# Kernel optimization log

Measured on AMD Instinct MI355X. Metric: run time of the kernel, lower is better.

## Reference

```python
import jax, jax.numpy as jnp
import numpy as np
import math

B, T, D = 1, 4096, 1024
H = 16
HD = D // H  # 64


def _rotate_half(x):
    d = x.shape[-1] // 2
    return jnp.concatenate([-x[..., d:], x[..., :d]], axis=-1)


def setup_inputs() -> dict:
    key = jax.random.key(0)
    k1, k2, k3 = jax.random.split(key, 3)
    x = jax.random.normal(k1, (B, T, D), dtype=jnp.float32)
    # Linear weights stored as (in, out) so forward is x @ W
    w_qkv = jax.random.normal(k2, (D, 3 * D), dtype=jnp.float32) * (1.0 / math.sqrt(D))
    w_proj = jax.random.normal(k3, (D, D), dtype=jnp.float32) * (1.0 / math.sqrt(D))
    return {"x": x, "w_qkv": w_qkv, "w_proj": w_proj}


def reference(x, w_qkv, w_proj):
    b, t, c = x.shape
    qkv = x @ w_qkv  # [b,t,3c]
    q, k, v = jnp.split(qkv, 3, axis=-1)
    # [b,h,t,hd]
    q = q.reshape(b, t, H, HD).transpose(0, 2, 1, 3)
    k = k.reshape(b, t, H, HD).transpose(0, 2, 1, 3)
    v = v.reshape(b, t, H, HD).transpose(0, 2, 1, 3)

    # RoPE (rotate_half style)
    inv_freq = 1.0 / (10000.0 ** (jnp.arange(0, HD, 2, dtype=jnp.float32) / HD))
    pos = jnp.arange(t, dtype=jnp.float32)
    freqs = jnp.outer(pos, inv_freq)            # [t, hd/2]
    cos = jnp.concatenate([jnp.cos(freqs), jnp.cos(freqs)], axis=-1)[None, None]  # [1,1,t,hd]
    sin = jnp.concatenate([jnp.sin(freqs), jnp.sin(freqs)], axis=-1)[None, None]
    q = q * cos + _rotate_half(q) * sin
    k = k * cos + _rotate_half(k) * sin

    att = jnp.einsum('bhqd,bhkd->bhqk', q, k) / math.sqrt(HD)  # [b,h,t,t]
    causal = jnp.tril(jnp.ones((t, t), dtype=bool))
    att = jnp.where(causal, att, -jnp.inf)
    att = jax.nn.softmax(att, axis=-1)
    # dropout is identity in eval mode
    y = jnp.einsum('bhqk,bhkd->bhqd', att, v)
    y = y.transpose(0, 2, 1, 3).reshape(b, t, c)
    return y @ w_proj
```

## Files before the change

kernel.cpp:

```cpp
#include <hip/hip_runtime.h>
#include <hip/hip_fp16.h>
#include <math.h>

#define TT 4096
#define DD 1024
#define NH 16
#define HD 64

typedef __attribute__((ext_vector_type(8))) _Float16 half8v;
typedef __attribute__((ext_vector_type(4))) _Float16 half4v;
typedef __attribute__((ext_vector_type(4))) float f32x4;

#define GLDS16(g, l)                                                        \
    __builtin_amdgcn_global_load_lds(                                       \
        (const __attribute__((address_space(1))) void*)(g),                 \
        (__attribute__((address_space(3))) void*)(l), 16, 0, 0)

__global__ __launch_bounds__(256) void cast_x(const float* __restrict__ X,
                                              _Float16* __restrict__ Xh)
{
    const int i = (blockIdx.x * 256 + threadIdx.x) * 8;
    float4 a = *(const float4*)&X[i];
    float4 b = *(const float4*)&X[i + 4];
    half8v o = {(_Float16)a.x, (_Float16)a.y, (_Float16)a.z, (_Float16)a.w,
                (_Float16)b.x, (_Float16)b.y, (_Float16)b.z, (_Float16)b.w};
    *(half8v*)&Xh[i] = o;
}

__global__ __launch_bounds__(256) void transpose_cast(
    const float* __restrict__ W, _Float16* __restrict__ WT, int K, int N)
{
    __shared__ float tile[64][65];
    const int t = threadIdx.x;
    const int k0 = blockIdx.y * 64, n0 = blockIdx.x * 64;
    const int c = (t & 15) * 4, r = t >> 4;
#pragma unroll
    for (int i = 0; i < 4; i++) {
        float4 v = *(const float4*)&W[(size_t)(k0 + r + 16 * i) * N + n0 + c];
        tile[r + 16 * i][c + 0] = v.x;
        tile[r + 16 * i][c + 1] = v.y;
        tile[r + 16 * i][c + 2] = v.z;
        tile[r + 16 * i][c + 3] = v.w;
    }
    __syncthreads();
#pragma unroll
    for (int i = 0; i < 4; i++) {
        const int n = r + 16 * i;
        half4v o;
        o[0] = (_Float16)tile[c + 0][n];
        o[1] = (_Float16)tile[c + 1][n];
        o[2] = (_Float16)tile[c + 2][n];
        o[3] = (_Float16)tile[c + 3][n];
        *(half4v*)&WT[(size_t)(n0 + n) * K + k0 + c] = o;
    }
}

template <int MODE>
__global__ __launch_bounds__(256) void gemm_h(
    const _Float16* __restrict__ A, const _Float16* __restrict__ Bt,
    float* __restrict__ C0, _Float16* __restrict__ Q,
    _Float16* __restrict__ Kk, _Float16* __restrict__ V,
    int M, int N, int K)
{
    __shared__ _Float16 As[128 * 32];
    __shared__ _Float16 Bs[128 * 32];
    const int tid  = threadIdx.x;
    const int wave = tid >> 6;
    const int lane = tid & 63;
    const int quad = lane >> 4;
    const int n16  = lane & 15;
    const int n0 = blockIdx.x * 128;
    const int m0 = blockIdx.y * 128;
    const int wr = (wave & 1) * 64;
    const int wc = (wave >> 1) * 64;

    f32x4 acc[4][4];
#pragma unroll
    for (int i = 0; i < 4; i++)
#pragma unroll
        for (int j = 0; j < 4; j++) acc[i][j] = (f32x4){0.f, 0.f, 0.f, 0.f};

    const int srow = tid >> 2;
    const int scol = (tid & 3) * 8;
    const _Float16* Ag = A + (size_t)(m0 + srow) * K + scol;
    const _Float16* Bg = Bt + (size_t)(n0 + srow) * K + scol;
    _Float16* AsW = As + (size_t)wave * 512;
    _Float16* BsW = Bs + (size_t)wave * 512;

    for (int k0 = 0; k0 < K; k0 += 32) {
        __syncthreads();
        GLDS16(Ag + k0, AsW);
        GLDS16(Ag + (size_t)64 * K + k0, AsW + 2048);
        GLDS16(Bg + k0, BsW);
        GLDS16(Bg + (size_t)64 * K + k0, BsW + 2048);
        __syncthreads();

        half8v aF[4], bF[4];
#pragma unroll
        for (int i = 0; i < 4; i++)
            aF[i] = *(const half8v*)&As[(size_t)(wr + i * 16 + n16) * 32 + quad * 8];
#pragma unroll
        for (int j = 0; j < 4; j++)
            bF[j] = *(const half8v*)&Bs[(size_t)(wc + j * 16 + n16) * 32 + quad * 8];
#pragma unroll
        for (int i = 0; i < 4; i++)
#pragma unroll
            for (int j = 0; j < 4; j++)
                acc[i][j] = __builtin_amdgcn_mfma_f32_16x16x32_f16(
                    aF[i], bF[j], acc[i][j], 0, 0, 0);
    }

    if (MODE == 0) {
#pragma unroll
        for (int i = 0; i < 4; i++)
#pragma unroll
            for (int j = 0; j < 4; j++)
#pragma unroll
                for (int r = 0; r < 4; r++) {
                    const int m = m0 + wr + i * 16 + quad * 4 + r;
                    const int n = n0 + wc + j * 16 + n16;
                    C0[(size_t)m * N + n] = acc[i][j][r];
                }
    } else {
        const int ncol0 = n0 + wc;
        const int which = ncol0 >> 10;
        const int h = (ncol0 & 1023) >> 6;
        if (which < 2) {
            _Float16* dst = (which == 0) ? Q : Kk;
            const float sc = (which == 0) ? 0.125f * 1.44269504f : 1.0f;
            const float K2 = 0.4152410118609203f;
#pragma unroll
            for (int jlo = 0; jlo < 2; jlo++) {
                const int d = jlo * 16 + n16;
                const float invf = exp2f(-(float)d * K2);
#pragma unroll
                for (int i = 0; i < 4; i++) {
#pragma unroll
                    for (int r = 0; r < 4; r++) {
                        const int t = m0 + wr + i * 16 + quad * 4 + r;
                        const float f = (float)t * invf;
                        float sn, cs;
                        __sincosf(f, &sn, &cs);
                        const float lo = acc[i][jlo][r];
                        const float hi = acc[i][jlo + 2][r];
                        const size_t off = ((size_t)h * TT + t) * HD + d;
                        dst[off]      = (_Float16)((lo * cs - hi * sn) * sc);
                        dst[off + 32] = (_Float16)((hi * cs + lo * sn) * sc);
                    }
                }
            }
        } else {
#pragma unroll
            for (int i = 0; i < 4; i++)
#pragma unroll
                for (int j = 0; j < 4; j++)
#pragma unroll
                    for (int r = 0; r < 4; r++) {
                        const int t = m0 + wr + i * 16 + quad * 4 + r;
                        const int d = j * 16 + n16;
                        const int cp = 2 * (t & 15) + ((t >> 4) & 1);
                        V[(((size_t)h * (TT / 32) + (t >> 5)) * 64 + d) * 32 + cp] =
                            (_Float16)acc[i][j][r];
                    }
        }
    }
}

__global__ __launch_bounds__(256) void zero_acc(float4* __restrict__ O4,
                                                float4* __restrict__ L4)
{
    const int i = blockIdx.x * 256 + threadIdx.x;
    const float4 z = {0.f, 0.f, 0.f, 0.f};
    O4[i] = z;
    if (i < 16384) L4[i] = z;
}

__global__ __launch_bounds__(256) void attn_kernel(
    const _Float16* __restrict__ Qh, const _Float16* __restrict__ Kh,
    const _Float16* __restrict__ Vp, _Float16* __restrict__ Oacc,
    float* __restrict__ Lacc)
{
    __shared__ _Float16 Ks[2][32][32];
    __shared__ _Float16 Vs[64][32];
    __shared__ _Float16 Ps[4][32][40];

    const int tid  = threadIdx.x;
    const int wave = tid >> 6;
    const int lane = tid & 63;
    const int quad = lane >> 4;
    const int n16  = lane & 15;
    const int h  = blockIdx.z;
    const int qt = 31 - blockIdx.y;
    const int s  = blockIdx.x;
    const int nT = 4 * qt + 4;
    const int nS = (qt + 4) >> 2;
    if (s >= nS) return;
    const int t_beg = s * nT / nS;
    const int t_end = (s + 1) * nT / nS;

    const int q0 = qt * 128;
    const int rowbase = q0 + wave * 32;

    const _Float16* Qg = Qh + (size_t)h * TT * HD;
    const _Float16* Kg = Kh + (size_t)h * TT * HD;
    const _Float16* Vg = Vp + (size_t)h * (TT / 32) * 2048;

    half8v aQ[2][2];
#pragma unroll
    for (int g = 0; g < 2; g++) {
        const int row = rowbase + g * 16 + n16;
#pragma unroll
        for (int c = 0; c < 2; c++)
            aQ[g][c] = *(const half8v*)(Qg + (size_t)row * HD + c * 32 + quad * 8);
    }

    f32x4 O[2][4], Ol[2];
#pragma unroll
    for (int g = 0; g < 2; g++) {
#pragma unroll
        for (int d = 0; d < 4; d++) O[g][d] = (f32x4){0.f, 0.f, 0.f, 0.f};
        Ol[g] = (f32x4){0.f, 0.f, 0.f, 0.f};
    }
    const half8v vOnes = {(_Float16)1, (_Float16)1, (_Float16)1, (_Float16)1,
                          (_Float16)1, (_Float16)1, (_Float16)1, (_Float16)1};

    const int kc = tid >> 7, kj = (tid >> 2) & 31, ks = tid & 3;
    const _Float16* kSrc = Kg + (size_t)kj * HD + kc * 32 + ks * 8;
    const _Float16* vSrc = Vg + (size_t)tid * 8;
    _Float16* ksBase = &Ks[0][0][0] + (size_t)wave * 512;
    _Float16* vsBase = &Vs[0][0] + (size_t)wave * 512;

    for (int it = t_beg; it < t_end; ++it) {
        const int j0 = it * 32;
        __syncthreads();
        GLDS16(kSrc + (size_t)j0 * HD, ksBase);
        GLDS16(vSrc + (size_t)it * 2048, vsBase);
        __syncthreads();

        if (j0 <= rowbase + 31) {
            const bool needMask = (j0 + 31 > rowbase);

            f32x4 S[2][2];
#pragma unroll
            for (int g = 0; g < 2; g++)
#pragma unroll
                for (int st = 0; st < 2; st++) {
                    S[g][st] = (f32x4){0.f, 0.f, 0.f, 0.f};
#pragma unroll
                    for (int c = 0; c < 2; c++) {
                        half8v bK = *(const half8v*)&Ks[c][st * 16 + n16][quad * 8];
                        S[g][st] = __builtin_amdgcn_mfma_f32_16x16x32_f16(
                            aQ[g][c], bK, S[g][st], 0, 0, 0);
                    }
                }

#pragma unroll
            for (int g = 0; g < 2; g++)
#pragma unroll
                for (int r = 0; r < 4; r++) {
                    const int row = rowbase + g * 16 + quad * 4 + r;
                    float x0 = S[g][0][r];
                    float x1 = S[g][1][r];
                    if (needMask) {
                        x0 = (j0 + n16      <= row) ? x0 : -1e30f;
                        x1 = (j0 + 16 + n16 <= row) ? x1 : -1e30f;
                    }
                    const float p0 = __builtin_amdgcn_exp2f(x0);
                    const float p1 = __builtin_amdgcn_exp2f(x1);
                    *(__half2*)&Ps[wave][g * 16 + quad * 4 + r][2 * n16] =
                        __floats2half2_rn(p0, p1);
                }

            half8v bV[4];
#pragma unroll
            for (int d = 0; d < 4; d++)
                bV[d] = *(const half8v*)&Vs[d * 16 + n16][quad * 8];
#pragma unroll
            for (int g = 0; g < 2; g++) {
                half8v aP = *(const half8v*)&Ps[wave][g * 16 + n16][quad * 8];
#pragma unroll
                for (int d = 0; d < 4; d++)
                    O[g][d] = __builtin_amdgcn_mfma_f32_16x16x32_f16(
                        aP, bV[d], O[g][d], 0, 0, 0);
                Ol[g] = __builtin_amdgcn_mfma_f32_16x16x32_f16(
                    aP, vOnes, Ol[g], 0, 0, 0);
            }
        }
    }

#pragma unroll
    for (int g = 0; g < 2; g++)
#pragma unroll
        for (int r = 0; r < 4; r++) {
            const int row = rowbase + g * 16 + quad * 4 + r;
            if (n16 == 0)
                unsafeAtomicAdd(&Lacc[h * TT + row], Ol[g][r]);
#pragma unroll
            for (int d = 0; d < 4; d++) {
                float v = O[g][d][r];
                float vn = __shfl_xor(v, 1);
                if ((lane & 1) == 0) {
                    __half2* dst = (__half2*)(Oacc +
                        ((size_t)h * TT + row) * HD + d * 16 + n16);
                    unsafeAtomicAdd(dst, __floats2half2_rn(v, vn));
                }
            }
        }
}

__global__ __launch_bounds__(256) void finalize(
    const _Float16* __restrict__ Oacc, const float* __restrict__ Lacc,
    _Float16* __restrict__ Y)
{
    const int gid = blockIdx.x * 256 + threadIdx.x;
    const int h = gid >> 15;
    const int rem = gid & 32767;
    const int t = rem >> 3;
    const int c = rem & 7;
    const float inv = 1.0f / Lacc[h * TT + t];
    half8v o = *(const half8v*)(Oacc + ((size_t)h * TT + t) * HD + c * 8);
    half8v y;
#pragma unroll
    for (int e = 0; e < 8; e++) y[e] = (_Float16)((float)o[e] * inv);
    *(half8v*)(Y + (size_t)t * DD + h * HD + c * 8) = y;
}

extern "C" void kernel_launch(void* const* d_in, const int* in_sizes, int n_in,
                              void* d_out, int out_size, void* d_ws, size_t ws_size,
                              hipStream_t stream)
{
    const float* x      = (const float*)d_in[0];
    const float* w_qkv  = (const float*)d_in[1];
    const float* w_proj = (const float*)d_in[2];
    float* out = (float*)d_out;

    char* ws = (char*)d_ws;
    const size_t MB = 1u << 20;
    _Float16* xh   = (_Float16*)(ws);
    _Float16* WqT  = (_Float16*)(ws + 8 * MB);
    _Float16* WpT  = (_Float16*)(ws + 14 * MB);
    _Float16* Qh   = (_Float16*)(ws + 16 * MB);
    _Float16* Kh   = (_Float16*)(ws + 24 * MB);
    _Float16* Vp   = (_Float16*)(ws + 32 * MB);
    _Float16* Yh   = (_Float16*)(ws + 40 * MB);
    _Float16* Oacc = (_Float16*)(ws + 48 * MB);
    float*    Lacc = (float*)(ws + 57 * MB);

    dim3 blk(256);

    cast_x<<<(TT * DD) / (256 * 8), blk, 0, stream>>>(x, xh);
    transpose_cast<<<dim3(3072 / 64, DD / 64), blk, 0, stream>>>(w_qkv, WqT, DD, 3 * DD);
    transpose_cast<<<dim3(DD / 64, DD / 64), blk, 0, stream>>>(w_proj, WpT, DD, DD);

    gemm_h<1><<<dim3(3072 / 128, TT / 128), blk, 0, stream>>>(
        xh, WqT, nullptr, Qh, Kh, Vp, TT, 3 * DD, DD);

    zero_acc<<<2048, blk, 0, stream>>>((float4*)Oacc, (float4*)Lacc);

    attn_kernel<<<dim3(8, 32, NH), blk, 0, stream>>>(Qh, Kh, Vp, Oacc, Lacc);

    finalize<<<2048, blk, 0, stream>>>(Oacc, Lacc, Yh);

    gemm_h<0><<<dim3(DD / 128, TT / 128), blk, 0, stream>>>(
        Yh, WpT, out, nullptr, nullptr, nullptr, TT, DD, DD);
}
```

Measured before the change: 280.7 us.

## Swizzle LDS tiles, vectorize V stores, fuse zeroing, halve attention splits

Applies an XOR swizzle to the 16-byte chunk index in LDS for the GEMM A/B tiles and the attention K/V tiles, aiming to cut bank conflicts on half8 fragment reads. The V epilogue now writes packed half8 vectors instead of scattered scalar halves. The accumulator zeroing moves into the x-cast kernel, removing one launch. Attention uses about half as many KV splits per query tile, with a smaller grid, which means fewer atomic partial accumulations but less parallelism.

```diff
diff --git a/kernel.cpp b/kernel.cpp
--- a/kernel.cpp
+++ b/kernel.cpp
@@ -16,15 +16,20 @@
         (const __attribute__((address_space(1))) void*)(g),                 \
         (__attribute__((address_space(3))) void*)(l), 16, 0, 0)
 
-__global__ __launch_bounds__(256) void cast_x(const float* __restrict__ X,
-                                              _Float16* __restrict__ Xh)
-{
-    const int i = (blockIdx.x * 256 + threadIdx.x) * 8;
+__global__ __launch_bounds__(256) void cast_x_zero(
+    const float* __restrict__ X, _Float16* __restrict__ Xh,
+    float4* __restrict__ O4, float4* __restrict__ L4)
+{
+    const int t = blockIdx.x * 256 + threadIdx.x;
+    const int i = t * 8;
     float4 a = *(const float4*)&X[i];
     float4 b = *(const float4*)&X[i + 4];
     half8v o = {(_Float16)a.x, (_Float16)a.y, (_Float16)a.z, (_Float16)a.w,
                 (_Float16)b.x, (_Float16)b.y, (_Float16)b.z, (_Float16)b.w};
     *(half8v*)&Xh[i] = o;
+    const float4 z = {0.f, 0.f, 0.f, 0.f};
+    O4[t] = z;
+    if (t < 16384) L4[t] = z;
 }
 
 __global__ __launch_bounds__(256) void transpose_cast(
@@ -81,11 +86,13 @@
         for (int j = 0; j < 4; j++) acc[i][j] = (f32x4){0.f, 0.f, 0.f, 0.f};
 
     const int srow = tid >> 2;
-    const int scol = (tid & 3) * 8;
-    const _Float16* Ag = A + (size_t)(m0 + srow) * K + scol;
-    const _Float16* Bg = Bt + (size_t)(n0 + srow) * K + scol;
+    const int schk = tid & 3;
+    const int sswz = (schk ^ ((srow >> 1) & 3)) * 8;
+    const _Float16* Ag = A + (size_t)(m0 + srow) * K + sswz;
+    const _Float16* Bg = Bt + (size_t)(n0 + srow) * K + sswz;
     _Float16* AsW = As + (size_t)wave * 512;
     _Float16* BsW = Bs + (size_t)wave * 512;
+    const int slot = (quad ^ ((n16 >> 1) & 3)) * 8;
 
     for (int k0 = 0; k0 < K; k0 += 32) {
         __syncthreads();
@@ -98,10 +105,10 @@
         half8v aF[4], bF[4];
 #pragma unroll
         for (int i = 0; i < 4; i++)
-            aF[i] = *(const half8v*)&As[(size_t)(wr + i * 16 + n16) * 32 + quad * 8];
+            aF[i] = *(const half8v*)&As[(size_t)(wr + i * 16 + n16) * 32 + slot];
 #pragma unroll
         for (int j = 0; j < 4; j++)
-            bF[j] = *(const half8v*)&Bs[(size_t)(wc + j * 16 + n16) * 32 + quad * 8];
+            bF[j] = *(const half8v*)&Bs[(size_t)(wc + j * 16 + n16) * 32 + slot];
 #pragma unroll
         for (int i = 0; i < 4; i++)
 #pragma unroll
@@ -151,28 +158,23 @@
             }
         } else {
 #pragma unroll
-            for (int i = 0; i < 4; i++)
-#pragma unroll
-                for (int j = 0; j < 4; j++)
+            for (int kb2 = 0; kb2 < 2; kb2++) {
+                const int kbg = ((m0 + wr) >> 5) + kb2;
+#pragma unroll
+                for (int j = 0; j < 4; j++) {
+                    const int d = j * 16 + n16;
+                    half8v o;
 #pragma unroll
                     for (int r = 0; r < 4; r++) {
-                        const int t = m0 + wr + i * 16 + quad * 4 + r;
-                        const int d = j * 16 + n16;
-                        const int cp = 2 * (t & 15) + ((t >> 4) & 1);
-                        V[(((size_t)h * (TT / 32) + (t >> 5)) * 64 + d) * 32 + cp] =
-                            (_Float16)acc[i][j][r];
+                        o[2 * r]     = (_Float16)acc[2 * kb2][j][r];
+                        o[2 * r + 1] = (_Float16)acc[2 * kb2 + 1][j][r];
                     }
+                    *(half8v*)(V + (((size_t)h * (TT / 32) + kbg) * 64 + d) * 32
+                               + quad * 8) = o;
+                }
+            }
         }
     }
-}
-
-__global__ __launch_bounds__(256) void zero_acc(float4* __restrict__ O4,
-                                                float4* __restrict__ L4)
-{
-    const int i = blockIdx.x * 256 + threadIdx.x;
-    const float4 z = {0.f, 0.f, 0.f, 0.f};
-    O4[i] = z;
-    if (i < 16384) L4[i] = z;
 }
 
 __global__ __launch_bounds__(256) void attn_kernel(
@@ -193,7 +195,7 @@
     const int qt = 31 - blockIdx.y;
     const int s  = blockIdx.x;
     const int nT = 4 * qt + 4;
-    const int nS = (qt + 4) >> 2;
+    const int nS = (qt + 8) >> 3;
     if (s >= nS) return;
     const int t_beg = s * nT / nS;
     const int t_end = (s + 1) * nT / nS;
@@ -225,10 +227,14 @@
                           (_Float16)1, (_Float16)1, (_Float16)1, (_Float16)1};
 
     const int kc = tid >> 7, kj = (tid >> 2) & 31, ks = tid & 3;
-    const _Float16* kSrc = Kg + (size_t)kj * HD + kc * 32 + ks * 8;
-    const _Float16* vSrc = Vg + (size_t)tid * 8;
+    const _Float16* kSrc = Kg + (size_t)kj * HD + kc * 32
+                           + (size_t)(ks ^ ((kj >> 1) & 3)) * 8;
+    const int vd = tid >> 2, vs = tid & 3;
+    const _Float16* vSrc = Vg + (size_t)vd * 32
+                           + (size_t)(vs ^ ((vd >> 1) & 3)) * 8;
     _Float16* ksBase = &Ks[0][0][0] + (size_t)wave * 512;
     _Float16* vsBase = &Vs[0][0] + (size_t)wave * 512;
+    const int slot = (quad ^ ((n16 >> 1) & 3)) * 8;
 
     for (int it = t_beg; it < t_end; ++it) {
         const int j0 = it * 32;
@@ -248,7 +254,7 @@
                     S[g][st] = (f32x4){0.f, 0.f, 0.f, 0.f};
 #pragma unroll
                     for (int c = 0; c < 2; c++) {
-                        half8v bK = *(const half8v*)&Ks[c][st * 16 + n16][quad * 8];
+                        half8v bK = *(const half8v*)&Ks[c][st * 16 + n16][slot];
                         S[g][st] = __builtin_amdgcn_mfma_f32_16x16x32_f16(
                             aQ[g][c], bK, S[g][st], 0, 0, 0);
                     }
@@ -274,7 +280,7 @@
             half8v bV[4];
 #pragma unroll
             for (int d = 0; d < 4; d++)
-                bV[d] = *(const half8v*)&Vs[d * 16 + n16][quad * 8];
+                bV[d] = *(const half8v*)&Vs[d * 16 + n16][slot];
 #pragma unroll
             for (int g = 0; g < 2; g++) {
                 half8v aP = *(const half8v*)&Ps[wave][g * 16 + n16][quad * 8];
@@ -348,16 +354,14 @@
 
     dim3 blk(256);
 
-    cast_x<<<(TT * DD) / (256 * 8), blk, 0, stream>>>(x, xh);
+    cast_x_zero<<<2048, blk, 0, stream>>>(x, xh, (float4*)Oacc, (float4*)Lacc);
     transpose_cast<<<dim3(3072 / 64, DD / 64), blk, 0, stream>>>(w_qkv, WqT, DD, 3 * DD);
     transpose_cast<<<dim3(DD / 64, DD / 64), blk, 0, stream>>>(w_proj, WpT, DD, DD);
 
     gemm_h<1><<<dim3(3072 / 128, TT / 128), blk, 0, stream>>>(
         xh, WqT, nullptr, Qh, Kh, Vp, TT, 3 * DD, DD);
 
-    zero_acc<<<2048, blk, 0, stream>>>((float4*)Oacc, (float4*)Lacc);
-
-    attn_kernel<<<dim3(8, 32, NH), blk, 0, stream>>>(Qh, Kh, Vp, Oacc, Lacc);
+    attn_kernel<<<dim3(4, 32, NH), blk, 0, stream>>>(Qh, Kh, Vp, Oacc, Lacc);
 
     finalize<<<2048, blk, 0, stream>>>(Oacc, Lacc, Yh);
 
```

Result: faster. 263.6 us (-6.1%).
